# Kernel tuning notes

Measured on AMD Instinct MI355X. Metric: run time of the kernel, lower is better.

## Reference

```python
import jax, jax.numpy as jnp
import numpy as np

B, S, D_IN, D_OUT = 4, 2048, 4096, 11008


def setup_inputs() -> dict:
    key = jax.random.key(0)
    kx, kw, ks, kb = jax.random.split(key, 4)
    x = jax.random.normal(kx, (B, S, D_IN), dtype=jnp.float32)
    # Simulate fp8 storage: values are exactly representable in float8_e4m3fn.
    w_raw = jax.random.normal(kw, (D_OUT, D_IN), dtype=jnp.float32)
    w_q = w_raw.astype(jnp.float8_e4m3fn).astype(jnp.float32)
    # Per-output-channel dequant scale (positive).
    scale = jax.random.uniform(ks, (D_OUT, 1), dtype=jnp.float32, minval=0.01, maxval=0.1)
    bias = jax.random.normal(kb, (D_OUT,), dtype=jnp.float32)
    return {"x": x, "w_q": w_q, "scale": scale, "bias": bias}


def reference(x, w_q, scale, bias):
    # dequantize_tensor: fp8 payload * per-channel scale -> full-precision weight [D_OUT, D_IN]
    w = w_q * scale
    # F.linear(x, w, bias) = x @ w.T + bias
    out = jnp.einsum('bsd,od->bso', x, w) + bias
    return out
```

## Files before the change

### kernel.cpp

```cpp
#include <hip/hip_runtime.h>
#include <hip/hip_bf16.h>
#include <stdint.h>

#define M_DIM 8192
#define N_DIM 11008
#define K_DIM 4096
#define BM 256
#define BN 256
#define BK 32
#define NT (K_DIM / BK)
#define NBX (N_DIM / BN)
#define NBY (M_DIM / BM)
#define NBLK (NBX * NBY)
#define CPX (NBLK / 8)

typedef __bf16 bf16_8 __attribute__((ext_vector_type(8)));
typedef float f32x4 __attribute__((ext_vector_type(4)));

__device__ __forceinline__ uint32_t pack_bf2(float lo, float hi) {
    uint32_t ulo = __float_as_uint(lo);
    uint32_t uhi = __float_as_uint(hi);
    ulo = (ulo + 0x7fffu + ((ulo >> 16) & 1u)) >> 16;
    uhi = (uhi + 0x7fffu + ((uhi >> 16) & 1u)) >> 16;
    return ulo | (uhi << 16);
}

__global__ __launch_bounds__(256) void cvt_f32_bf16(const float* __restrict__ src,
                                                    uint2* __restrict__ dst, int n4) {
    int i = blockIdx.x * 256 + threadIdx.x;
    if (i >= n4) return;
    float4 a = ((const float4*)src)[i];
    uint2 o;
    o.x = pack_bf2(a.x, a.y);
    o.y = pack_bf2(a.z, a.w);
    dst[i] = o;
}

__device__ __forceinline__ void load_lds16(const __bf16* g, __bf16* l) {
    __builtin_amdgcn_global_load_lds(
        (__attribute__((address_space(1))) void*)(g),
        (__attribute__((address_space(3))) void*)(l),
        16, 0, 0);
}

#define VMCNT(n) asm volatile("s_waitcnt vmcnt(" #n ")" ::: "memory")
#define LGKM0    asm volatile("s_waitcnt lgkmcnt(0)" ::: "memory")
#define SCHED0   __builtin_amdgcn_sched_barrier(0)

__device__ __forceinline__ void wg_barrier() {
    asm volatile("" ::: "memory");
    __builtin_amdgcn_s_barrier();
    asm volatile("" ::: "memory");
}

__device__ __forceinline__ void stage_pair(const __bf16* G, __bf16* L, int wave, long ko) {
    __bf16* lw = L + wave * 16 * BK;
    load_lds16(G + ko, lw);
    load_lds16(G + 128L * K_DIM + ko, lw + 128 * BK);
}

__global__ __launch_bounds__(512, 2) void gemm_bt_scaled(
    const __bf16* __restrict__ A, const __bf16* __restrict__ W,
    const float* __restrict__ scale, const float* __restrict__ bias,
    float* __restrict__ C) {
    __shared__ __align__(16) __bf16 As[4][BM * BK];
    __shared__ __align__(16) __bf16 Bs[4][BN * BK];

    const int t = threadIdx.x;
    const int wave = t >> 6;
    const int lane = t & 63;
    const int wm = wave >> 2;
    const int wn = wave & 3;

    const int bid = (int)blockIdx.x;
    const int swz = (bid & 7) * CPX + (bid >> 3);
    const int by = swz / NBX;
    const int bx = swz - by * NBX;
    const int m0 = by * BM;
    const int n0 = bx * BN;

    const int srow = lane >> 2;
    const int sch = ((lane & 3) ^ ((lane >> 3) & 3)) * 8;
    const __bf16* Ag = A + (long)(m0 + wave * 16 + srow) * K_DIM + sch;
    const __bf16* Wg = W + (long)(n0 + wave * 16 + srow) * K_DIM + sch;

    const int lrow = lane & 15;
    const int swzr = (lrow >> 1) & 3;
    const int lk = ((lane >> 4) ^ swzr) * 8;
    const int aoff = (wm * 128 + lrow) * BK + lk;
    const int boff = (wn * 64 + lrow) * BK + lk;

    f32x4 acc[8][4] = {};

    stage_pair(Ag, &As[0][0], wave, 0);
    stage_pair(Wg, &Bs[0][0], wave, 0);
    stage_pair(Ag, &As[1][0], wave, (long)BK);
    stage_pair(Wg, &Bs[1][0], wave, (long)BK);
    stage_pair(Ag, &As[2][0], wave, 2L * BK);
    stage_pair(Wg, &Bs[2][0], wave, 2L * BK);
    VMCNT(8);
    wg_barrier();

    int tt = 0;
    for (; tt < NT - 3; ++tt) {
        const int sl = tt & 3;
        const int sn = (tt + 3) & 3;
        const long ko = (long)(tt + 3) * BK;
        const __bf16* Ab = &As[sl][aoff];
        const __bf16* Bb = &Bs[sl][boff];

        bf16_8 a0[4], bv[4];
#pragma unroll
        for (int i = 0; i < 4; i++) a0[i] = *(const bf16_8*)(Ab + i * 16 * BK);
#pragma unroll
        for (int j = 0; j < 4; j++) bv[j] = *(const bf16_8*)(Bb + j * 16 * BK);
        stage_pair(Ag, &As[sn][0], wave, ko);
        wg_barrier();
        LGKM0;
        SCHED0;
        __builtin_amdgcn_s_setprio(1);
#pragma unroll
        for (int i = 0; i < 4; i++)
#pragma unroll
            for (int j = 0; j < 4; j++)
                acc[i][j] = __builtin_amdgcn_mfma_f32_16x16x32_bf16(a0[i], bv[j], acc[i][j], 0, 0, 0);
        __builtin_amdgcn_s_setprio(0);
        SCHED0;
        wg_barrier();

        bf16_8 a1[4];
#pragma unroll
        for (int i = 0; i < 4; i++) a1[i] = *(const bf16_8*)(Ab + (4 + i) * 16 * BK);
        stage_pair(Wg, &Bs[sn][0], wave, ko);
        wg_barrier();
        LGKM0;
        SCHED0;
        __builtin_amdgcn_s_setprio(1);
#pragma unroll
        for (int i = 0; i < 4; i++)
#pragma unroll
            for (int j = 0; j < 4; j++)
                acc[4 + i][j] = __builtin_amdgcn_mfma_f32_16x16x32_bf16(a1[i], bv[j], acc[4 + i][j], 0, 0, 0);
        __builtin_amdgcn_s_setprio(0);
        SCHED0;
        VMCNT(8);
        wg_barrier();
    }

#pragma unroll 1
    for (int e = 0; e < 3; ++e) {
        const int sl = (tt + e) & 3;
        const __bf16* Ab = &As[sl][aoff];
        const __bf16* Bb = &Bs[sl][boff];
        bf16_8 af[8], bv[4];
#pragma unroll
        for (int i = 0; i < 8; i++) af[i] = *(const bf16_8*)(Ab + i * 16 * BK);
#pragma unroll
        for (int j = 0; j < 4; j++) bv[j] = *(const bf16_8*)(Bb + j * 16 * BK);
        __builtin_amdgcn_s_setprio(1);
#pragma unroll
        for (int i = 0; i < 8; i++)
#pragma unroll
            for (int j = 0; j < 4; j++)
                acc[i][j] = __builtin_amdgcn_mfma_f32_16x16x32_bf16(af[i], bv[j], acc[i][j], 0, 0, 0);
        __builtin_amdgcn_s_setprio(0);
        if (e == 0) { VMCNT(4); wg_barrier(); }
        else if (e == 1) { VMCNT(0); wg_barrier(); }
    }

    const int crow4 = (lane >> 4) * 4;
    const int ccol = lane & 15;
#pragma unroll
    for (int j = 0; j < 4; j++) {
        const int n = n0 + wn * 64 + j * 16 + ccol;
        const float sc = scale[n];
        const float bi = bias[n];
#pragma unroll
        for (int i = 0; i < 8; i++) {
            const int mbase = m0 + wm * 128 + i * 16 + crow4;
#pragma unroll
            for (int r = 0; r < 4; r++) {
                C[(long)(mbase + r) * N_DIM + n] = acc[i][j][r] * sc + bi;
            }
        }
    }
}

extern "C" void kernel_launch(void* const* d_in, const int* in_sizes, int n_in,
                              void* d_out, int out_size, void* d_ws, size_t ws_size,
                              hipStream_t stream) {
    const float* x = (const float*)d_in[0];
    const float* w_q = (const float*)d_in[1];
    const float* scale = (const float*)d_in[2];
    const float* bias = (const float*)d_in[3];
    float* out = (float*)d_out;

    __bf16* x_bf = (__bf16*)d_ws;
    __bf16* w_bf = (__bf16*)((char*)d_ws + (size_t)M_DIM * K_DIM * sizeof(__bf16));

    const int n4x = (M_DIM * K_DIM) / 4;
    const int n4w = (N_DIM * K_DIM) / 4;
    cvt_f32_bf16<<<(n4x + 255) / 256, 256, 0, stream>>>(x, (uint2*)x_bf, n4x);
    cvt_f32_bf16<<<(n4w + 255) / 256, 256, 0, stream>>>(w_q, (uint2*)w_bf, n4w);

    gemm_bt_scaled<<<dim3(NBLK), 512, 0, stream>>>(x_bf, w_bf, scale, bias, out);
}
```

Baseline: 1.441 ms.

## Prefetch next k-tile LDS fragments into registers during MFMA phases

Restructures the GEMM main loop into a templated k-step that loads the next tile's A/B fragments from LDS into ping-pong register buffers while the current tile's second MFMA half runs. It uses partial lgkmcnt waits and drops one of the three barriers per k-step, and the epilogue is folded into the same step function. The aim is to hide LDS read latency behind matrix-core work and cut synchronisation. In exchange it raises register pressure (two sets of fragment buffers) at 2 waves/SIMD occupancy, and the vmcnt/barrier ordering is more delicate to get right.

```diff
diff --git a/kernel.cpp b/kernel.cpp
--- a/kernel.cpp
+++ b/kernel.cpp
@@ -9,6 +9,7 @@
 #define BN 256
 #define BK 32
 #define NT (K_DIM / BK)
+#define TSLOT (BM * BK)
 #define NBX (N_DIM / BN)
 #define NBY (M_DIM / BM)
 #define NBLK (NBX * NBY)
@@ -44,7 +45,7 @@
 }
 
 #define VMCNT(n) asm volatile("s_waitcnt vmcnt(" #n ")" ::: "memory")
-#define LGKM0    asm volatile("s_waitcnt lgkmcnt(0)" ::: "memory")
+#define LGKM(n)  asm volatile("s_waitcnt lgkmcnt(" #n ")" ::: "memory")
 #define SCHED0   __builtin_amdgcn_sched_barrier(0)
 
 __device__ __forceinline__ void wg_barrier() {
@@ -59,12 +60,68 @@
     load_lds16(G + 128L * K_DIM + ko, lw + 128 * BK);
 }
 
+template <bool HAS_NEXT>
+__device__ __forceinline__ void kstep(
+    int tt, const __bf16* AsB, const __bf16* BsB, __bf16* AsW, __bf16* BsW,
+    int aoff, int boff, const __bf16* Ag, const __bf16* Wg, int wave,
+    bf16_8 (&a0)[4], bf16_8 (&bv)[4],
+    bf16_8 (&a0n)[4], bf16_8 (&bvn)[4],
+    bf16_8 (&a1)[4],
+    f32x4 (&acc)[8][4]) {
+    const int sl = tt & 3;
+    const __bf16* Ab = AsB + sl * TSLOT + aoff;
+    const __bf16* Bb = BsB + sl * TSLOT + boff;
+    const bool doStage = (tt + 3) < NT;
+    const int sn = (tt + 3) & 3;
+    const long ko = (long)(tt + 3) * BK;
+
+    if (doStage) stage_pair(Ag, AsW + sn * TSLOT, wave, ko);
+#pragma unroll
+    for (int i = 0; i < 4; i++) a1[i] = *(const bf16_8*)(Ab + (4 + i) * 16 * BK);
+    wg_barrier();
+    LGKM(4);
+    SCHED0;
+    __builtin_amdgcn_s_setprio(1);
+#pragma unroll
+    for (int i = 0; i < 4; i++)
+#pragma unroll
+        for (int j = 0; j < 4; j++)
+            acc[i][j] = __builtin_amdgcn_mfma_f32_16x16x32_bf16(a0[i], bv[j], acc[i][j], 0, 0, 0);
+    __builtin_amdgcn_s_setprio(0);
+
+    if (doStage) stage_pair(Wg, BsW + sn * TSLOT, wave, ko);
+    if (HAS_NEXT) {
+        const int sl1 = (tt + 1) & 3;
+        const __bf16* Abn = AsB + sl1 * TSLOT + aoff;
+        const __bf16* Bbn = BsB + sl1 * TSLOT + boff;
+#pragma unroll
+        for (int i = 0; i < 4; i++) a0n[i] = *(const bf16_8*)(Abn + i * 16 * BK);
+#pragma unroll
+        for (int j = 0; j < 4; j++) bvn[j] = *(const bf16_8*)(Bbn + j * 16 * BK);
+        LGKM(8);
+    } else {
+        LGKM(0);
+    }
+    SCHED0;
+    __builtin_amdgcn_s_setprio(1);
+#pragma unroll
+    for (int i = 0; i < 4; i++)
+#pragma unroll
+        for (int j = 0; j < 4; j++)
+            acc[4 + i][j] = __builtin_amdgcn_mfma_f32_16x16x32_bf16(a1[i], bv[j], acc[4 + i][j], 0, 0, 0);
+    __builtin_amdgcn_s_setprio(0);
+
+    if (tt < NT - 3) { VMCNT(4); }
+    else if (tt == NT - 3) { VMCNT(0); }
+    wg_barrier();
+}
+
 __global__ __launch_bounds__(512, 2) void gemm_bt_scaled(
     const __bf16* __restrict__ A, const __bf16* __restrict__ W,
     const float* __restrict__ scale, const float* __restrict__ bias,
     float* __restrict__ C) {
-    __shared__ __align__(16) __bf16 As[4][BM * BK];
-    __shared__ __align__(16) __bf16 Bs[4][BN * BK];
+    __shared__ __align__(16) __bf16 As[4][TSLOT];
+    __shared__ __align__(16) __bf16 Bs[4][TSLOT];
 
     const int t = threadIdx.x;
     const int wave = t >> 6;
@@ -90,83 +147,42 @@
     const int aoff = (wm * 128 + lrow) * BK + lk;
     const int boff = (wn * 64 + lrow) * BK + lk;
 
+    const __bf16* AsB = &As[0][0];
+    const __bf16* BsB = &Bs[0][0];
+    __bf16* AsW = &As[0][0];
+    __bf16* BsW = &Bs[0][0];
+
     f32x4 acc[8][4] = {};
-
-    stage_pair(Ag, &As[0][0], wave, 0);
-    stage_pair(Wg, &Bs[0][0], wave, 0);
-    stage_pair(Ag, &As[1][0], wave, (long)BK);
-    stage_pair(Wg, &Bs[1][0], wave, (long)BK);
-    stage_pair(Ag, &As[2][0], wave, 2L * BK);
-    stage_pair(Wg, &Bs[2][0], wave, 2L * BK);
+    bf16_8 a0A[4], bvA[4], a0B[4], bvB[4], a1[4];
+
+    stage_pair(Ag, AsW + 0 * TSLOT, wave, 0);
+    stage_pair(Wg, BsW + 0 * TSLOT, wave, 0);
+    stage_pair(Ag, AsW + 1 * TSLOT, wave, (long)BK);
+    stage_pair(Wg, BsW + 1 * TSLOT, wave, (long)BK);
+    stage_pair(Ag, AsW + 2 * TSLOT, wave, 2L * BK);
+    stage_pair(Wg, BsW + 2 * TSLOT, wave, 2L * BK);
     VMCNT(8);
     wg_barrier();
+#pragma unroll
+    for (int i = 0; i < 4; i++) a0A[i] = *(const bf16_8*)(AsB + aoff + i * 16 * BK);
+#pragma unroll
+    for (int j = 0; j < 4; j++) bvA[j] = *(const bf16_8*)(BsB + boff + j * 16 * BK);
 
     int tt = 0;
-    for (; tt < NT - 3; ++tt) {
-        const int sl = tt & 3;
-        const int sn = (tt + 3) & 3;
-        const long ko = (long)(tt + 3) * BK;
-        const __bf16* Ab = &As[sl][aoff];
-        const __bf16* Bb = &Bs[sl][boff];
-
-        bf16_8 a0[4], bv[4];
-#pragma unroll
-        for (int i = 0; i < 4; i++) a0[i] = *(const bf16_8*)(Ab + i * 16 * BK);
-#pragma unroll
-        for (int j = 0; j < 4; j++) bv[j] = *(const bf16_8*)(Bb + j * 16 * BK);
-        stage_pair(Ag, &As[sn][0], wave, ko);
-        wg_barrier();
-        LGKM0;
-        SCHED0;
-        __builtin_amdgcn_s_setprio(1);
-#pragma unroll
-        for (int i = 0; i < 4; i++)
-#pragma unroll
-            for (int j = 0; j < 4; j++)
-                acc[i][j] = __builtin_amdgcn_mfma_f32_16x16x32_bf16(a0[i], bv[j], acc[i][j], 0, 0, 0);
-        __builtin_amdgcn_s_setprio(0);
-        SCHED0;
-        wg_barrier();
-
-        bf16_8 a1[4];
-#pragma unroll
-        for (int i = 0; i < 4; i++) a1[i] = *(const bf16_8*)(Ab + (4 + i) * 16 * BK);
-        stage_pair(Wg, &Bs[sn][0], wave, ko);
-        wg_barrier();
-        LGKM0;
-        SCHED0;
-        __builtin_amdgcn_s_setprio(1);
-#pragma unroll
-        for (int i = 0; i < 4; i++)
-#pragma unroll
-            for (int j = 0; j < 4; j++)
-                acc[4 + i][j] = __builtin_amdgcn_mfma_f32_16x16x32_bf16(a1[i], bv[j], acc[4 + i][j], 0, 0, 0);
-        __builtin_amdgcn_s_setprio(0);
-        SCHED0;
-        VMCNT(8);
-        wg_barrier();
+#pragma unroll 1
+    for (int it = 0; it < (NT - 2) / 2; ++it) {
+        kstep<true>(tt, AsB, BsB, AsW, BsW, aoff, boff, Ag, Wg, wave,
+                    a0A, bvA, a0B, bvB, a1, acc);
+        ++tt;
+        kstep<true>(tt, AsB, BsB, AsW, BsW, aoff, boff, Ag, Wg, wave,
+                    a0B, bvB, a0A, bvA, a1, acc);
+        ++tt;
     }
-
-#pragma unroll 1
-    for (int e = 0; e < 3; ++e) {
-        const int sl = (tt + e) & 3;
-        const __bf16* Ab = &As[sl][aoff];
-        const __bf16* Bb = &Bs[sl][boff];
-        bf16_8 af[8], bv[4];
-#pragma unroll
-        for (int i = 0; i < 8; i++) af[i] = *(const bf16_8*)(Ab + i * 16 * BK);
-#pragma unroll
-        for (int j = 0; j < 4; j++) bv[j] = *(const bf16_8*)(Bb + j * 16 * BK);
-        __builtin_amdgcn_s_setprio(1);
-#pragma unroll
-        for (int i = 0; i < 8; i++)
-#pragma unroll
-            for (int j = 0; j < 4; j++)
-                acc[i][j] = __builtin_amdgcn_mfma_f32_16x16x32_bf16(af[i], bv[j], acc[i][j], 0, 0, 0);
-        __builtin_amdgcn_s_setprio(0);
-        if (e == 0) { VMCNT(4); wg_barrier(); }
-        else if (e == 1) { VMCNT(0); wg_barrier(); }
-    }
+    kstep<true>(tt, AsB, BsB, AsW, BsW, aoff, boff, Ag, Wg, wave,
+                a0A, bvA, a0B, bvB, a1, acc);
+    ++tt;
+    kstep<false>(tt, AsB, BsB, AsW, BsW, aoff, boff, Ag, Wg, wave,
+                 a0B, bvB, a0A, bvA, a1, acc);
 
     const int crow4 = (lane >> 4) * 4;
     const int ccol = lane & 15;
```

Measured after the change: 1.418 ms. Within noise of the previous version (-1.6%).
